# Optimization experiments

Measured on AMD Instinct MI355X. Metric: run time of the kernel, lower is better.

## Reference

```python
import jax, jax.numpy as jnp
import numpy as np

EPS = 1e-5  # clamp floor on learnable input scale (elastic quantizer)


def setup_inputs() -> dict:
    key = jax.random.key(0)
    k0, k1, k2, k3 = jax.random.split(key, 4)
    B, S, H = 8, 4096, 1024
    hidden_states = jax.random.normal(k0, (B, S, H), dtype=jnp.float32)
    W = jax.random.normal(k1, (H, H), dtype=jnp.float32) * 0.02
    b = jax.random.normal(k2, (H,), dtype=jnp.float32) * 0.02
    alpha = jax.random.uniform(k3, (1,), dtype=jnp.float32) + 0.1  # learnable input scale
    return {"hidden_states": hidden_states, "W": W, "b": b, "alpha": alpha}


def reference(hidden_states, W, b, alpha):
    # index_select first token along dim=-2 -> [B, 1, H]
    first_token = hidden_states[..., 0:1, :]
    # elastic 1-bit signed input quantization: x_q = sign(x) * alpha (alpha clamped)
    a = jnp.maximum(alpha, EPS)
    x_q = jnp.sign(first_token) * a
    # BWN weight quantization (layerwise): w_q = sign(W) * mean(|W|)
    w_scale = jnp.mean(jnp.abs(W))
    w_q = jnp.sign(W) * w_scale
    # linear: y = x_q @ w_q^T + b, then tanh
    out = jnp.einsum('bsh,oh->bso', x_q, w_q) + b
    return jnp.tanh(out)
```

## Files before the change

### kernel.cpp

```cpp
#include <hip/hip_runtime.h>
#include <math.h>

#define HDIM 1024
#define BATCH 8
#define SEQ 4096


__global__ __launch_bounds__(256) void k1(const float* __restrict__ hs,
                                          const float* __restrict__ W,
                                          float* __restrict__ wpart,
                                          int* __restrict__ dotp) {
    const int tid = threadIdx.x;
    const int wave = tid >> 6, lane = tid & 63;
    const int gw = blockIdx.x * 4 + wave;
    const int o = gw & (HDIM - 1);
    const int part = gw >> 10;
    const int h0 = part * 256 + lane * 4;

    float4 wv = *reinterpret_cast<const float4*>(W + (size_t)o * HDIM + h0);
    const float we[4] = {wv.x, wv.y, wv.z, wv.w};

    float xe[BATCH][4];
    #pragma unroll
    for (int b = 0; b < BATCH; ++b) {
        float4 xv = *reinterpret_cast<const float4*>(hs + (size_t)b * SEQ * HDIM + h0);
        xe[b][0] = xv.x; xe[b][1] = xv.y; xe[b][2] = xv.z; xe[b][3] = xv.w;
    }

    float aabs = 0.f;
    int n[BATCH], d[BATCH];
    #pragma unroll
    for (int b = 0; b < BATCH; ++b) { n[b] = 0; d[b] = 0; }

    #pragma unroll
    for (int j = 0; j < 4; ++j) {
        unsigned long long wsg = __ballot(we[j] < 0.f);
        unsigned long long wnz = __ballot(we[j] != 0.f);
        aabs += fabsf(we[j]);
        #pragma unroll
        for (int b = 0; b < BATCH; ++b) {
            unsigned long long u = wnz & __ballot(xe[b][j] != 0.f);
            unsigned long long m = (wsg ^ __ballot(xe[b][j] < 0.f)) & u;
            n[b] += __popcll(u);
            d[b] += __popcll(m);
        }
    }

    #pragma unroll
    for (int off = 32; off >= 1; off >>= 1) aabs += __shfl_down(aabs, off, 64);
    if (lane == 0) {
        wpart[gw] = aabs;
        #pragma unroll
        for (int b = 0; b < BATCH; ++b)
            dotp[(part * BATCH + b) * HDIM + o] = n[b] - 2 * d[b];
    }
}

__global__ __launch_bounds__(256) void k2(const int* __restrict__ dotp,
                                          const float* __restrict__ wpart,
                                          const float* __restrict__ bias,
                                          const float* __restrict__ alpha,
                                          float* __restrict__ out) {
    __shared__ float red[256];
    const int tid = threadIdx.x;
    float s = 0.f;
    #pragma unroll
    for (int i = 0; i < 16; ++i) s += wpart[tid + i * 256];
    red[tid] = s;
    __syncthreads();
    #pragma unroll
    for (int off = 128; off >= 1; off >>= 1) {
        if (tid < off) red[tid] += red[tid + off];
        __syncthreads();
    }
    float a = alpha[0];
    if (a < 1e-5f) a = 1e-5f;
    const float scale = a * red[0] * (1.0f / 1048576.0f);

    const int idx = blockIdx.x * 256 + tid;
    const int b = idx >> 10, o = idx & (HDIM - 1);
    int dsum = dotp[(0 * BATCH + b) * HDIM + o]
             + dotp[(1 * BATCH + b) * HDIM + o]
             + dotp[(2 * BATCH + b) * HDIM + o]
             + dotp[(3 * BATCH + b) * HDIM + o];
    out[idx] = tanhf(scale * (float)dsum + bias[o]);
}

extern "C" void kernel_launch(void* const* d_in, const int* in_sizes, int n_in,
                              void* d_out, int out_size, void* d_ws, size_t ws_size,
                              hipStream_t stream) {
    const float* hs    = (const float*)d_in[0];
    const float* W     = (const float*)d_in[1];
    const float* bias  = (const float*)d_in[2];
    const float* alpha = (const float*)d_in[3];
    float* out = (float*)d_out;

    float* wpart = (float*)d_ws;
    int* dotp = (int*)(wpart + 4096);

    k1<<<1024, 256, 0, stream>>>(hs, W, wpart, dotp);
    k2<<<(BATCH * HDIM) / 256, 256, 0, stream>>>(dotp, wpart, bias, alpha, out);
}
```

Baseline: 12.05 us.

## Fuse two kernels into one with flag-based grid sync and last-stage block 0

Merges the partial-dot kernel and the reduce/tanh kernel into a single launch. Each block publishes its partials with agent-scope atomic stores and raises a tagged flag, and block 0 spins on all flags, reduces the weight-abs sum, then computes all 8192 outputs by itself and resets the flags. This removes one kernel launch and the gap between the two kernels. In exchange, the final stage is serialized onto one block, and it relies on block 0 staying resident while it spins and on the flags in the workspace starting at zero.

Result: slower. 26.61 us (+120.8%).

```diff
diff --git a/kernel.cpp b/kernel.cpp
--- a/kernel.cpp
+++ b/kernel.cpp
@@ -4,12 +4,18 @@
 #define HDIM 1024
 #define BATCH 8
 #define SEQ 4096
+#define NBLK 1024
+#define TAG 0x51CAFE77u
 
 
-__global__ __launch_bounds__(256) void k1(const float* __restrict__ hs,
-                                          const float* __restrict__ W,
-                                          float* __restrict__ wpart,
-                                          int* __restrict__ dotp) {
+__global__ __launch_bounds__(256) void k_all(const float* __restrict__ hs,
+                                             const float* __restrict__ W,
+                                             const float* __restrict__ bias,
+                                             const float* __restrict__ alpha,
+                                             float* __restrict__ out,
+                                             unsigned int* __restrict__ flags,
+                                             float* __restrict__ wpart,
+                                             int* __restrict__ dotp) {
     const int tid = threadIdx.x;
     const int wave = tid >> 6, lane = tid & 63;
     const int gw = blockIdx.x * 4 + wave;
@@ -19,7 +25,6 @@
 
     float4 wv = *reinterpret_cast<const float4*>(W + (size_t)o * HDIM + h0);
     const float we[4] = {wv.x, wv.y, wv.z, wv.w};
-
     float xe[BATCH][4];
     #pragma unroll
     for (int b = 0; b < BATCH; ++b) {
@@ -31,7 +36,6 @@
     int n[BATCH], d[BATCH];
     #pragma unroll
     for (int b = 0; b < BATCH; ++b) { n[b] = 0; d[b] = 0; }
-
     #pragma unroll
     for (int j = 0; j < 4; ++j) {
         unsigned long long wsg = __ballot(we[j] < 0.f);
@@ -45,27 +49,36 @@
             d[b] += __popcll(m);
         }
     }
-
     #pragma unroll
     for (int off = 32; off >= 1; off >>= 1) aabs += __shfl_down(aabs, off, 64);
+
     if (lane == 0) {
-        wpart[gw] = aabs;
+        __hip_atomic_store(&wpart[gw], aabs, __ATOMIC_RELAXED, __HIP_MEMORY_SCOPE_AGENT);
         #pragma unroll
         for (int b = 0; b < BATCH; ++b)
-            dotp[(part * BATCH + b) * HDIM + o] = n[b] - 2 * d[b];
+            __hip_atomic_store(&dotp[(part * BATCH + b) * HDIM + o], n[b] - 2 * d[b],
+                               __ATOMIC_RELAXED, __HIP_MEMORY_SCOPE_AGENT);
     }
-}
+    asm volatile("s_waitcnt vmcnt(0)" ::: "memory");
+    __syncthreads();
+    if (tid == 0)
+        __hip_atomic_store(&flags[blockIdx.x], TAG, __ATOMIC_RELAXED, __HIP_MEMORY_SCOPE_AGENT);
 
-__global__ __launch_bounds__(256) void k2(const int* __restrict__ dotp,
-                                          const float* __restrict__ wpart,
-                                          const float* __restrict__ bias,
-                                          const float* __restrict__ alpha,
-                                          float* __restrict__ out) {
+    if (blockIdx.x != 0) return;
+
     __shared__ float red[256];
-    const int tid = threadIdx.x;
+    #pragma unroll
+    for (int i = 0; i < NBLK / 256; ++i) {
+        while (__hip_atomic_load(&flags[tid * (NBLK / 256) + i],
+                                 __ATOMIC_RELAXED, __HIP_MEMORY_SCOPE_AGENT) != TAG)
+            __builtin_amdgcn_s_sleep(4);
+    }
+    __syncthreads();
+
     float s = 0.f;
     #pragma unroll
-    for (int i = 0; i < 16; ++i) s += wpart[tid + i * 256];
+    for (int i = 0; i < 16; ++i)
+        s += __hip_atomic_load(&wpart[tid + i * 256], __ATOMIC_RELAXED, __HIP_MEMORY_SCOPE_AGENT);
     red[tid] = s;
     __syncthreads();
     #pragma unroll
@@ -77,13 +90,22 @@
     if (a < 1e-5f) a = 1e-5f;
     const float scale = a * red[0] * (1.0f / 1048576.0f);
 
-    const int idx = blockIdx.x * 256 + tid;
-    const int b = idx >> 10, o = idx & (HDIM - 1);
-    int dsum = dotp[(0 * BATCH + b) * HDIM + o]
-             + dotp[(1 * BATCH + b) * HDIM + o]
-             + dotp[(2 * BATCH + b) * HDIM + o]
-             + dotp[(3 * BATCH + b) * HDIM + o];
-    out[idx] = tanhf(scale * (float)dsum + bias[o]);
+    #pragma unroll
+    for (int i = 0; i < 32; ++i) {
+        const int idx = i * 256 + tid;
+        const int b = idx >> 10, oo = idx & (HDIM - 1);
+        int dsum = 0;
+        #pragma unroll
+        for (int p = 0; p < 4; ++p)
+            dsum += __hip_atomic_load(&dotp[(p * BATCH + b) * HDIM + oo],
+                                      __ATOMIC_RELAXED, __HIP_MEMORY_SCOPE_AGENT);
+        out[idx] = tanhf(scale * (float)dsum + bias[oo]);
+    }
+
+    #pragma unroll
+    for (int i = 0; i < NBLK / 256; ++i)
+        __hip_atomic_store(&flags[tid * (NBLK / 256) + i], 0u,
+                           __ATOMIC_RELAXED, __HIP_MEMORY_SCOPE_AGENT);
 }
 
 extern "C" void kernel_launch(void* const* d_in, const int* in_sizes, int n_in,
@@ -95,9 +117,9 @@
     const float* alpha = (const float*)d_in[3];
     float* out = (float*)d_out;
 
-    float* wpart = (float*)d_ws;
+    unsigned int* flags = (unsigned int*)d_ws;
+    float* wpart = (float*)(flags + NBLK);
     int* dotp = (int*)(wpart + 4096);
 
-    k1<<<1024, 256, 0, stream>>>(hs, W, wpart, dotp);
-    k2<<<(BATCH * HDIM) / 256, 256, 0, stream>>>(dotp, wpart, bias, alpha, out);
+    k_all<<<NBLK, 256, 0, stream>>>(hs, W, bias, alpha, out, flags, wpart, dotp);
 }
```
